# Kernel tuning notes

Hardware: AMD Instinct MI355X
Metric: run time of the kernel (lower is better)

Reference implementation:

```python
import jax, jax.numpy as jnp
import numpy as np

NEG_SLOPE = 0.2
EPS = 1e-16  # PyG softmax denominator epsilon


def gat_conv(x, edge_index, W, a_src, a_dst, bias):
    """PyG GATConv, heads=1, concat=True, add_self_loops=True, edge_dim=None."""
    N = x.shape[0]
    h = x @ W  # [N, d]
    loops = jnp.arange(N)
    src = jnp.concatenate([edge_index[0], loops])  # [E+N]
    dst = jnp.concatenate([edge_index[1], loops])
    # per-node attention dot-products, gathered per edge
    s = h @ a_src  # [N]
    t = h @ a_dst  # [N]
    e = jax.nn.leaky_relu(s[src] + t[dst], NEG_SLOPE)  # [E+N]
    # segment softmax over incoming edges of each dst node
    m = jax.ops.segment_max(e, dst, num_segments=N)
    ex = jnp.exp(e - m[dst])
    denom = jax.ops.segment_sum(ex, dst, num_segments=N)
    alpha = ex / (denom[dst] + EPS)  # [E+N]
    out = jax.ops.segment_sum(h[src] * alpha[:, None], dst, num_segments=N)
    return out + bias


def setup_inputs() -> dict:
    key = jax.random.key(0)
    N, E, D, DE = 50000, 600000, 128, 16
    ks = jax.random.split(key, 12)
    scale = 1.0 / np.sqrt(D)
    return {
        "x_one": jax.random.normal(ks[0], (N, D), jnp.float32),
        "edge_index_one": jax.random.randint(ks[1], (2, E), 0, N, jnp.int64),
        "edge_attr_emb_one": jax.random.normal(ks[2], (E, DE), jnp.float32),
        "x_two": jax.random.normal(ks[3], (N, D), jnp.float32),
        "edge_index_two": jax.random.randint(ks[4], (2, E), 0, N, jnp.int64),
        "edge_attr_emb_two": jax.random.normal(ks[5], (E, DE), jnp.float32),
        "W1": jax.random.normal(ks[6], (D, D), jnp.float32) * scale,
        "a_src1": jax.random.normal(ks[7], (D,), jnp.float32) * scale,
        "a_dst1": jax.random.normal(ks[8], (D,), jnp.float32) * scale,
        "b1": jnp.zeros((D,), jnp.float32),
        "W2": jax.random.normal(ks[9], (D, D), jnp.float32) * scale,
        "a_src2": jax.random.normal(ks[10], (D,), jnp.float32) * scale,
        "a_dst2": jax.random.normal(ks[11], (D,), jnp.float32) * scale,
        "b2": jnp.zeros((D,), jnp.float32),
    }


def reference(x_one, edge_index_one, edge_attr_emb_one,
              x_two, edge_index_two, edge_attr_emb_two,
              W1, a_src1, a_dst1, b1, W2, a_src2, a_dst2, b2):
    # edge_attr is ignored: GATConv was built without edge_dim.
    # F.dropout(training=False) is identity in eval mode.
    out_one = jax.nn.relu(gat_conv(x_one, edge_index_one, W1, a_src1, a_dst1, b1))
    out_two = jax.nn.relu(gat_conv(x_two, edge_index_two, W2, a_src2, a_dst2, b2))
    return (out_one, out_two)
```

## Files before the change

kernel.cpp:

```cpp
#include <hip/hip_runtime.h>
#include <math.h>

#define D 128
#define NEG_SLOPE 0.2f
#define EPS 1e-16f
#define PT 4096
#define SCAP 1024
#define SLOTS 64
#define SSTR 66
#define UCS 64

typedef __attribute__((ext_vector_type(8))) __bf16 bf16x8;
typedef __attribute__((ext_vector_type(4))) float f32x4;
typedef __attribute__((ext_vector_type(2))) float f32x2;

__device__ __forceinline__ unsigned short f2bf(float f) {
    return __builtin_bit_cast(unsigned short, (__bf16)f);
}
__device__ __forceinline__ unsigned long long pack4bf(float a, float b, float c, float d) {
    return (unsigned long long)f2bf(a)
         | ((unsigned long long)f2bf(b) << 16)
         | ((unsigned long long)f2bf(c) << 32)
         | ((unsigned long long)f2bf(d) << 48);
}
__device__ __forceinline__ f32x2 bf2f2(unsigned u) {
    f32x2 r;
    r.x = __uint_as_float(u << 16);
    r.y = __uint_as_float(u & 0xffff0000u);
    return r;
}

__global__ __launch_bounds__(256) void k_fused(const float* __restrict__ X0,
                                               const float* __restrict__ X1,
                                               const float* __restrict__ W0,
                                               const float* __restrict__ W1,
                                               const float* __restrict__ as0,
                                               const float* __restrict__ as1,
                                               const float* __restrict__ ad0,
                                               const float* __restrict__ ad1,
                                               unsigned short* __restrict__ Hb,
                                               float* __restrict__ sv,
                                               float* __restrict__ tv,
                                               const int* __restrict__ s0,
                                               const int* __restrict__ d0,
                                               const int* __restrict__ s1,
                                               const int* __restrict__ d1,
                                               int* __restrict__ ucnt,
                                               unsigned* __restrict__ P,
                                               int N, int nb, int npart,
                                               int E0, int Et, int NSB) {
    __shared__ char lds[32768];
    const int t = threadIdx.x;

    if (blockIdx.x < npart) {
        int* hcnt = (int*)lds;
        int* hbase = (int*)(lds + 8192);
        const int i0 = blockIdx.x * PT;
        const int i1 = min(i0 + PT, Et);
        for (int i = t; i < NSB; i += 256) hcnt[i] = 0;
        __syncthreads();
        for (int i = i0 + t; i < i1; i += 256) {
            int dd = (i < E0) ? d0[i] : d1[i - E0] + N;
            atomicAdd(&hcnt[dd >> 6], 1);
        }
        __syncthreads();
        for (int i = t; i < NSB; i += 256) {
            int c = hcnt[i];
            hbase[i] = c ? (i * SCAP + atomicAdd(&ucnt[(size_t)i * UCS], c)) : 0;
            hcnt[i] = 0;
        }
        __syncthreads();
        for (int i = i0 + t; i < i1; i += 256) {
            int ss, dd;
            if (i < E0) { ss = s0[i]; dd = d0[i]; }
            else        { ss = s1[i - E0] + N; dd = d1[i - E0] + N; }
            int sb = dd >> 6;
            int pos = hbase[sb] + atomicAdd(&hcnt[sb], 1);
            if (pos < (sb + 1) * SCAP)
                P[pos] = (unsigned)ss | ((unsigned)(dd & 63) << 26);
        }
        return;
    }

    const int gb = blockIdx.x - npart;
    const int g = (gb >= nb) ? 1 : 0;
    const int row0 = (gb - g * nb) * 128;
    const float* X = g ? X1 : X0;
    const float* W = g ? W1 : W0;
    const float* a_src = g ? as1 : as0;
    const float* a_dst = g ? ad1 : ad0;
    const int gbase = g * N;

    {
        const int n = t & 127;
        const int khalf = (t >> 7) * 64;
        #pragma unroll 4
        for (int i = 0; i < 16; ++i) {
            const int k0 = khalf + i * 4;
            float f0 = W[(size_t)(k0 + 0) * D + n];
            float f1 = W[(size_t)(k0 + 1) * D + n];
            float f2 = W[(size_t)(k0 + 2) * D + n];
            float f3 = W[(size_t)(k0 + 3) * D + n];
            int off = (n * 256 + k0 * 2) ^ ((n & 7) << 4);
            *(unsigned long long*)(lds + off) = pack4bf(f0, f1, f2, f3);
        }
    }
    __syncthreads();

    const int w = t >> 6;
    const int l = t & 63;
    const int lr = l & 15;
    const int lg = l >> 4;
    const int m0 = row0 + w * 32 + lr;
    const int m1 = m0 + 16;
    const float4* X4 = (const float4*)X;

    f32x4 acc[2][8];
    #pragma unroll
    for (int r = 0; r < 2; ++r)
        #pragma unroll
        for (int nt = 0; nt < 8; ++nt) acc[r][nt] = (f32x4){0.f, 0.f, 0.f, 0.f};

    #pragma unroll
    for (int kk = 0; kk < 4; ++kk) {
        const int kByte = kk * 64 + lg * 16;
        float4 xa0 = make_float4(0.f, 0.f, 0.f, 0.f), xa1 = xa0, xb0 = xa0, xb1 = xa0;
        const int fidx = kk * 8 + lg * 2;
        if (m0 < N) {
            xa0 = X4[(size_t)m0 * 32 + fidx];
            xa1 = X4[(size_t)m0 * 32 + fidx + 1];
        }
        if (m1 < N) {
            xb0 = X4[(size_t)m1 * 32 + fidx];
            xb1 = X4[(size_t)m1 * 32 + fidx + 1];
        }
        ulonglong2 ua, ub;
        ua.x = pack4bf(xa0.x, xa0.y, xa0.z, xa0.w);
        ua.y = pack4bf(xa1.x, xa1.y, xa1.z, xa1.w);
        ub.x = pack4bf(xb0.x, xb0.y, xb0.z, xb0.w);
        ub.y = pack4bf(xb1.x, xb1.y, xb1.z, xb1.w);
        bf16x8 a0 = __builtin_bit_cast(bf16x8, ua);
        bf16x8 a1 = __builtin_bit_cast(bf16x8, ub);
        #pragma unroll
        for (int nt = 0; nt < 8; ++nt) {
            const int n = nt * 16 + lr;
            bf16x8 b = *(const bf16x8*)(lds + ((n * 256 + kByte) ^ ((n & 7) << 4)));
            acc[0][nt] = __builtin_amdgcn_mfma_f32_16x16x32_bf16(a0, b, acc[0][nt], 0, 0, 0);
            acc[1][nt] = __builtin_amdgcn_mfma_f32_16x16x32_bf16(a1, b, acc[1][nt], 0, 0, 0);
        }
    }

    float asv[8], adv[8];
    #pragma unroll
    for (int nt = 0; nt < 8; ++nt) {
        asv[nt] = a_src[nt * 16 + lr];
        adv[nt] = a_dst[nt * 16 + lr];
    }
    #pragma unroll
    for (int r = 0; r < 2; ++r) {
        #pragma unroll
        for (int reg = 0; reg < 4; ++reg) {
            const int row = row0 + w * 32 + r * 16 + lg * 4 + reg;
            float ss = 0.f, tt = 0.f;
            #pragma unroll
            for (int nt = 0; nt < 8; ++nt) {
                float hv = acc[r][nt][reg];
                ss += hv * asv[nt];
                tt += hv * adv[nt];
                if (row < N) Hb[(size_t)(gbase + row) * D + nt * 16 + lr] = f2bf(hv);
            }
            #pragma unroll
            for (int off = 8; off; off >>= 1) {
                ss += __shfl_xor(ss, off);
                tt += __shfl_xor(tt, off);
            }
            if (lr == 0 && row < N) { sv[gbase + row] = ss; tv[gbase + row] = tt; }
        }
    }
}

__global__ __launch_bounds__(256) void k_gatherf(const unsigned* __restrict__ P,
                                                 const int* __restrict__ ucnt,
                                                 const float* __restrict__ sv,
                                                 const float* __restrict__ tv,
                                                 const unsigned short* __restrict__ Hb,
                                                 const float* __restrict__ b0,
                                                 const float* __restrict__ b1,
                                                 float* __restrict__ out, int N, int M) {
    __shared__ uint2 ep[32 * SSTR];
    __shared__ int cnt[32];
    __shared__ float tvl[32];
    const int t = threadIdx.x;
    const int pb = blockIdx.x >> 1;
    const int half = blockIdx.x & 1;
    const int dbase = blockIdx.x << 5;
    const int bstart = pb * SCAP;
    const int bend = bstart + min(ucnt[(size_t)pb * UCS], SCAP);

    if (t < 32) {
        int d = dbase + t;
        int dc = min(d, M - 1);
        float tvd = tv[dc];
        tvl[t] = tvd;
        float es = sv[dc] + tvd;
        es = (es > 0.f) ? es : NEG_SLOPE * es;
        float ps = __expf(es);
        bool ok = (d < M);
        ep[t * SSTR] = make_uint2((unsigned)dc, ok ? __float_as_uint(ps) : 0u);
        cnt[t] = 1;
    }
    __syncthreads();
    for (int i = bstart + t; i < bend; i += 256) {
        unsigned w = P[i];
        int dl6 = (int)(w >> 26);
        if ((dl6 >> 5) == half) {
            int dlo = dl6 & 31;
            int src = (int)(w & 0x03FFFFFFu);
            float e = sv[src] + tvl[dlo];
            e = (e > 0.f) ? e : NEG_SLOPE * e;
            float p = __expf(e);
            int pos = atomicAdd(&cnt[dlo], 1);
            if (pos < SLOTS) ep[dlo * SSTR + pos] = make_uint2((unsigned)src, __float_as_uint(p));
        }
    }
    __syncthreads();
    if (t < 32) {
        int c = min(cnt[t], SLOTS);
        int c4 = min((c + 3) & ~3, SLOTS);
        unsigned dsrc = (unsigned)min(dbase + t, M - 1);
        for (int k = c; k < c4; ++k) ep[t * SSTR + k] = make_uint2(dsrc, 0u);
        cnt[t] = c4;
    }
    __syncthreads();

    const int wv = t >> 6;
    const int lane = t & 63;
    const int qtr = lane >> 4;
    const int sl = lane & 15;
    const int qid = wv * 4 + qtr;

    #pragma unroll
    for (int r = 0; r < 2; ++r) {
        const int ld = qid + r * 16;
        const int d = dbase + ld;
        const int dg = cnt[ld];
        const int base = ld * SSTR;

        f32x2 a0 = {0.f, 0.f}, a1 = {0.f, 0.f}, a2 = {0.f, 0.f}, a3 = {0.f, 0.f};
        float sden = 0.f;
        for (int j = 0; j < dg; j += 4) {
            uint2 e0 = ep[base + j];
            uint2 e1 = ep[base + j + 1];
            uint2 e2 = ep[base + j + 2];
            uint2 e3 = ep[base + j + 3];
            float p0 = __uint_as_float(e0.y);
            float p1 = __uint_as_float(e1.y);
            float p2 = __uint_as_float(e2.y);
            float p3 = __uint_as_float(e3.y);
            sden += (p0 + p1) + (p2 + p3);
            uint4 w0 = *(const uint4*)(Hb + (size_t)e0.x * D + sl * 8);
            uint4 w1 = *(const uint4*)(Hb + (size_t)e1.x * D + sl * 8);
            uint4 w2 = *(const uint4*)(Hb + (size_t)e2.x * D + sl * 8);
            uint4 w3 = *(const uint4*)(Hb + (size_t)e3.x * D + sl * 8);
            a0 += p0 * bf2f2(w0.x); a1 += p0 * bf2f2(w0.y); a2 += p0 * bf2f2(w0.z); a3 += p0 * bf2f2(w0.w);
            a0 += p1 * bf2f2(w1.x); a1 += p1 * bf2f2(w1.y); a2 += p1 * bf2f2(w1.z); a3 += p1 * bf2f2(w1.w);
            a0 += p2 * bf2f2(w2.x); a1 += p2 * bf2f2(w2.y); a2 += p2 * bf2f2(w2.z); a3 += p2 * bf2f2(w2.w);
            a0 += p3 * bf2f2(w3.x); a1 += p3 * bf2f2(w3.y); a2 += p3 * bf2f2(w3.z); a3 += p3 * bf2f2(w3.w);
        }

        if (d < M) {
            const float* bp = ((d < N) ? b0 : b1) + sl * 8;
            float inv = 1.0f / (sden + EPS);
            float4 o0, o1;
            o0.x = fmaxf(a0.x * inv + bp[0], 0.f);
            o0.y = fmaxf(a0.y * inv + bp[1], 0.f);
            o0.z = fmaxf(a1.x * inv + bp[2], 0.f);
            o0.w = fmaxf(a1.y * inv + bp[3], 0.f);
            o1.x = fmaxf(a2.x * inv + bp[4], 0.f);
            o1.y = fmaxf(a2.y * inv + bp[5], 0.f);
            o1.z = fmaxf(a3.x * inv + bp[6], 0.f);
            o1.w = fmaxf(a3.y * inv + bp[7], 0.f);
            float4* op = (float4*)(out + (size_t)d * D + sl * 8);
            op[0] = o0;
            op[1] = o1;
        }
    }
}

static inline size_t rup(size_t x) { return (x + 255) & ~(size_t)255; }

extern "C" void kernel_launch(void* const* d_in, const int* in_sizes, int n_in,
                              void* d_out, int out_size, void* d_ws, size_t ws_size,
                              hipStream_t stream) {
    const int N = in_sizes[0] / D;
    const int M = 2 * N;
    const int E0 = in_sizes[1] / 2;
    const int E1 = in_sizes[4] / 2;
    const int Et = E0 + E1;
    const int NSB = (M + 63) >> 6;
    const int NGB = (M + 31) >> 5;
    const int NPART = (Et + PT - 1) / PT;
    float* out = (float*)d_out;

    char* ws = (char*)d_ws;
    unsigned short* Hb = (unsigned short*)ws; ws += rup((size_t)M * D * sizeof(unsigned short));
    float* sv = (float*)ws;       ws += rup((size_t)M * sizeof(float));
    float* tv = (float*)ws;       ws += rup((size_t)M * sizeof(float));
    int* ucnt = (int*)ws;         ws += rup((size_t)NSB * UCS * sizeof(int));
    unsigned* P = (unsigned*)ws;

    const int* EI0 = (const int*)d_in[1];
    const int* EI1 = (const int*)d_in[4];
    const int* s0 = EI0, *d0 = EI0 + E0;
    const int* s1 = EI1, *d1 = EI1 + E1;

    const int nb = (N + 127) / 128;

    hipMemsetAsync(ucnt, 0, (size_t)NSB * UCS * sizeof(int), stream);

    k_fused<<<NPART + 2 * nb, 256, 0, stream>>>(
        (const float*)d_in[0], (const float*)d_in[3],
        (const float*)d_in[6], (const float*)d_in[10],
        (const float*)d_in[7], (const float*)d_in[11],
        (const float*)d_in[8], (const float*)d_in[12],
        Hb, sv, tv, s0, d0, s1, d1, ucnt, P, N, nb, NPART, E0, Et, NSB);
    k_gatherf<<<NGB, 256, 0, stream>>>(P, ucnt, sv, tv, Hb,
                                       (const float*)d_in[9], (const float*)d_in[13],
                                       out, N, M);
}
```

Baseline: 95.62 us.

## Pre-transpose W to bf16 globally and stage X tile in LDS instead

A new tiny kernel converts and transposes each weight matrix to bf16 once per call. The GEMM blocks then stage their 128-row X tile in swizzled LDS with coalesced loads and read the B operand straight from the small global/L2-resident bf16 weight. This removes the strided per-block fp32 weight transpose and the uncoalesced per-lane X loads. The cost is an extra kernel launch on the critical path and B fragments coming from global memory on every MFMA step rather than from LDS.

```diff
diff --git a/kernel.cpp b/kernel.cpp
--- a/kernel.cpp
+++ b/kernel.cpp
@@ -30,10 +30,23 @@
     return r;
 }
 
+__global__ __launch_bounds__(256) void k_prew(const float* __restrict__ W0,
+                                              const float* __restrict__ W1,
+                                              unsigned short* __restrict__ Wt0,
+                                              unsigned short* __restrict__ Wt1) {
+    const float* W = blockIdx.x ? W1 : W0;
+    unsigned short* Wt = blockIdx.x ? Wt1 : Wt0;
+    for (int i = threadIdx.x; i < D * D; i += 256) {
+        int n = i >> 7;
+        int k = i & 127;
+        Wt[i] = f2bf(W[(size_t)k * D + n]);
+    }
+}
+
 __global__ __launch_bounds__(256) void k_fused(const float* __restrict__ X0,
                                                const float* __restrict__ X1,
-                                               const float* __restrict__ W0,
-                                               const float* __restrict__ W1,
+                                               const unsigned short* __restrict__ Wt0,
+                                               const unsigned short* __restrict__ Wt1,
                                                const float* __restrict__ as0,
                                                const float* __restrict__ as1,
                                                const float* __restrict__ ad0,
@@ -86,23 +99,22 @@
     const int g = (gb >= nb) ? 1 : 0;
     const int row0 = (gb - g * nb) * 128;
     const float* X = g ? X1 : X0;
-    const float* W = g ? W1 : W0;
+    const unsigned short* Wt = g ? Wt1 : Wt0;
     const float* a_src = g ? as1 : as0;
     const float* a_dst = g ? ad1 : ad0;
     const int gbase = g * N;
 
     {
-        const int n = t & 127;
-        const int khalf = (t >> 7) * 64;
+        const int c = t & 31;
+        const float4* X4 = (const float4*)X;
         #pragma unroll 4
-        for (int i = 0; i < 16; ++i) {
-            const int k0 = khalf + i * 4;
-            float f0 = W[(size_t)(k0 + 0) * D + n];
-            float f1 = W[(size_t)(k0 + 1) * D + n];
-            float f2 = W[(size_t)(k0 + 2) * D + n];
-            float f3 = W[(size_t)(k0 + 3) * D + n];
-            int off = (n * 256 + k0 * 2) ^ ((n & 7) << 4);
-            *(unsigned long long*)(lds + off) = pack4bf(f0, f1, f2, f3);
+        for (int p = 0; p < 16; ++p) {
+            const int m = p * 8 + (t >> 5);
+            const int gr = row0 + m;
+            float4 v = make_float4(0.f, 0.f, 0.f, 0.f);
+            if (gr < N) v = X4[(size_t)gr * 32 + c];
+            int off = (m * 256 + c * 8) ^ ((m & 7) << 4);
+            *(unsigned long long*)(lds + off) = pack4bf(v.x, v.y, v.z, v.w);
         }
     }
     __syncthreads();
@@ -111,9 +123,6 @@
     const int l = t & 63;
     const int lr = l & 15;
     const int lg = l >> 4;
-    const int m0 = row0 + w * 32 + lr;
-    const int m1 = m0 + 16;
-    const float4* X4 = (const float4*)X;
 
     f32x4 acc[2][8];
     #pragma unroll
@@ -124,27 +133,15 @@
     #pragma unroll
     for (int kk = 0; kk < 4; ++kk) {
         const int kByte = kk * 64 + lg * 16;
-        float4 xa0 = make_float4(0.f, 0.f, 0.f, 0.f), xa1 = xa0, xb0 = xa0, xb1 = xa0;
-        const int fidx = kk * 8 + lg * 2;
-        if (m0 < N) {
-            xa0 = X4[(size_t)m0 * 32 + fidx];
-            xa1 = X4[(size_t)m0 * 32 + fidx + 1];
-        }
-        if (m1 < N) {
-            xb0 = X4[(size_t)m1 * 32 + fidx];
-            xb1 = X4[(size_t)m1 * 32 + fidx + 1];
-        }
-        ulonglong2 ua, ub;
-        ua.x = pack4bf(xa0.x, xa0.y, xa0.z, xa0.w);
-        ua.y = pack4bf(xa1.x, xa1.y, xa1.z, xa1.w);
-        ub.x = pack4bf(xb0.x, xb0.y, xb0.z, xb0.w);
-        ub.y = pack4bf(xb1.x, xb1.y, xb1.z, xb1.w);
-        bf16x8 a0 = __builtin_bit_cast(bf16x8, ua);
-        bf16x8 a1 = __builtin_bit_cast(bf16x8, ub);
+        const int m0 = w * 32 + lr;
+        const int m1 = m0 + 16;
+        bf16x8 a0 = *(const bf16x8*)(lds + ((m0 * 256 + kByte) ^ ((m0 & 7) << 4)));
+        bf16x8 a1 = *(const bf16x8*)(lds + ((m1 * 256 + kByte) ^ ((m1 & 7) << 4)));
+        const int kElem = kk * 32 + lg * 8;
         #pragma unroll
         for (int nt = 0; nt < 8; ++nt) {
             const int n = nt * 16 + lr;
-            bf16x8 b = *(const bf16x8*)(lds + ((n * 256 + kByte) ^ ((n & 7) << 4)));
+            bf16x8 b = *(const bf16x8*)(Wt + (size_t)n * D + kElem);
             acc[0][nt] = __builtin_amdgcn_mfma_f32_16x16x32_bf16(a0, b, acc[0][nt], 0, 0, 0);
             acc[1][nt] = __builtin_amdgcn_mfma_f32_16x16x32_bf16(a1, b, acc[1][nt], 0, 0, 0);
         }
@@ -307,6 +304,8 @@
     float* sv = (float*)ws;       ws += rup((size_t)M * sizeof(float));
     float* tv = (float*)ws;       ws += rup((size_t)M * sizeof(float));
     int* ucnt = (int*)ws;         ws += rup((size_t)NSB * UCS * sizeof(int));
+    unsigned short* Wt0 = (unsigned short*)ws; ws += rup((size_t)D * D * sizeof(unsigned short));
+    unsigned short* Wt1 = (unsigned short*)ws; ws += rup((size_t)D * D * sizeof(unsigned short));
     unsigned* P = (unsigned*)ws;
 
     const int* EI0 = (const int*)d_in[1];
@@ -318,9 +317,11 @@
 
     hipMemsetAsync(ucnt, 0, (size_t)NSB * UCS * sizeof(int), stream);
 
+    k_prew<<<2, 256, 0, stream>>>((const float*)d_in[6], (const float*)d_in[10], Wt0, Wt1);
+
     k_fused<<<NPART + 2 * nb, 256, 0, stream>>>(
         (const float*)d_in[0], (const float*)d_in[3],
-        (const float*)d_in[6], (const float*)d_in[10],
+        Wt0, Wt1,
         (const float*)d_in[7], (const float*)d_in[11],
         (const float*)d_in[8], (const float*)d_in[12],
         Hb, sv, tv, s0, d0, s1, d1, ucnt, P, N, nb, NPART, E0, Et, NSB);
```

Measured after the change: 118.2 us. 23.6% more time.
